# Performance work log

Measured on AMD Instinct MI355X. Metric: run time of the kernel, lower is better.

The kernel has to match this reference:

```python
import jax, jax.numpy as jnp
import numpy as np

DIM = 256; CTX_DIM = 256; K = 7; SK = 5; NH = 4  # num_heads*2
HD = DIM // NH; SCALE = HD ** -0.5
H = 64; W = 64; HC = 56; WC = 56
LN_EPS = 1e-6; BN_EPS = 1e-5


def make_bias_idx(k, h, w):
    # Faithful port of ContMix.generate_idx + apply_rpb index construction.
    rs = 2 * k - 1
    idx_h = np.arange(k); idx_w = np.arange(k)
    idx_k = (idx_h[:, None] * rs + idx_w).reshape(-1)
    rep_h = np.ones(k, np.int64); rep_h[k // 2] = h - (k - 1)
    rep_w = np.ones(k, np.int64); rep_w[k // 2] = w - (k - 1)
    bias_hw = np.repeat(idx_h, rep_h)[:, None] * rs + np.repeat(idx_w, rep_w)  # (h, w)
    bias_idx = (bias_hw[..., None] + idx_k).reshape(-1, k * k)                 # (h*w, k^2)
    return jnp.asarray(bias_idx[::-1].copy())  # torch.flip along dim 0


def window_idx(n, k):
    # NATTEN-style clamped neighborhood window starts.
    s = np.clip(np.arange(n) - k // 2, 0, n - k)
    return jnp.asarray(s[:, None] + np.arange(k))  # (n, k)


BIDX1 = make_bias_idx(SK, H, W)
BIDX2 = make_bias_idx(K, H, W)
IDXI_S = window_idx(H, SK); IDXJ_S = window_idx(W, SK)
IDXI_L = window_idx(H, K);  IDXJ_L = window_idx(W, K)


def ln2d(x, g, b):
    # LayerNorm over channel dim per spatial location, x: (B, C, H, W)
    mu = x.mean(1, keepdims=True)
    var = ((x - mu) ** 2).mean(1, keepdims=True)
    return (x - mu) * jax.lax.rsqrt(var + LN_EPS) * g[None, :, None, None] + b[None, :, None, None]


def conv1x1(x, Wt):
    return jnp.einsum('oc,bchw->bohw', Wt, x)


def apply_rpb(attn, rpb, bias_idx, h, w):
    g = rpb.shape[0]
    r = rpb.reshape(g, -1)[:, bias_idx]  # (g, h*w, k^2)
    return attn + r.reshape(1, g, h, w, -1)


def na2d_av(attn, value, k, idx_i, idx_j):
    # attn: (B, G, H, W, k^2), value: (B, G, H, W, C)
    B, G, h, w, _ = attn.shape
    v = value[:, :, idx_i]        # (B, G, H, k, W, C)
    v = v[:, :, :, :, idx_j]      # (B, G, H, k, W, k, C)
    a = attn.reshape(B, G, h, w, k, k)
    return jnp.einsum('bghwpq,bghpwqc->bghwc', a, v)


def contmix_forward(x, ctx, Wq, gq, bq, Wk, gk, bk, Wproj, rpb1, rpb2, Wdy, bn_g, bn_b):
    B = x.shape[0]
    q = ln2d(conv1x1(x, Wq), gq, bq) * SCALE                       # (B, DIM, H, W)
    # AdaptiveAvgPool2d(7) on 56x56 -> exact 8x8 bins
    kctx = ctx.reshape(B, CTX_DIM, 7, HC // 7, 7, WC // 7).mean((3, 5))
    kf = ln2d(conv1x1(kctx, Wk), gk, bk)                            # (B, DIM, 7, 7)
    q = q.reshape(B, NH, HD, H * W)
    kf = kf.reshape(B, NH, HD, 49)
    wgt = jnp.einsum('bgcn,bgcl->bgnl', q, kf)                      # (B, 4, HW, 49)
    wgt = jnp.einsum('ml,bgnl->bgnm', Wproj, wgt)                   # (B, 4, HW, 74)
    wgt = wgt.reshape(B, NH, H, W, SK * SK + K * K)
    attn1 = wgt[:, :NH // 2, :, :, :SK * SK]                        # group1, 25
    attn2 = wgt[:, NH // 2:, :, :, SK * SK:]                        # group2, 49
    attn1 = jax.nn.softmax(apply_rpb(attn1, rpb1, BIDX1, H, W), -1)
    attn2 = jax.nn.softmax(apply_rpb(attn2, rpb2, BIDX2, H, W), -1)
    # 'b (m g c) h w -> m b g h w c', m=2, g=2
    v = x.reshape(B, 2, NH // 2, HD, H, W).transpose(1, 0, 2, 4, 5, 3)
    x1 = na2d_av(attn1, v[0], SK, IDXI_S, IDXJ_S)                   # (B, 2, H, W, HD)
    x2 = na2d_av(attn2, v[1], K, IDXI_L, IDXJ_L)
    out = jnp.concatenate([x1, x2], axis=1)                         # (B, 4, H, W, HD)
    out = out.transpose(0, 1, 4, 2, 3).reshape(B, DIM, H, W)
    out = conv1x1(out, Wdy)
    # BatchNorm2d in eval mode: running_mean=0, running_var=1
    out = out * (bn_g * jax.lax.rsqrt(jnp.float32(1.0) + BN_EPS))[None, :, None, None] + bn_b[None, :, None, None]
    return out


def setup_inputs() -> dict:
    key = jax.random.key(0)
    ks = jax.random.split(key, 10)
    d = {}
    d['x'] = jax.random.normal(ks[0], (4, DIM, H, W), jnp.float32)
    d['ctx'] = jax.random.normal(ks[1], (4, CTX_DIM, HC, WC), jnp.float32)
    d['Wq'] = jax.random.normal(ks[2], (DIM, DIM), jnp.float32) * 0.02
    d['gq'] = jnp.ones((DIM,), jnp.float32)
    d['bq'] = jnp.zeros((DIM,), jnp.float32)
    d['Wk'] = jax.random.normal(ks[3], (DIM, CTX_DIM), jnp.float32) * 0.02
    d['gk'] = jnp.ones((DIM,), jnp.float32)
    d['bk'] = jnp.zeros((DIM,), jnp.float32)
    d['Wproj'] = jax.random.normal(ks[4], (SK * SK + K * K, 49), jnp.float32) * 0.1
    d['rpb1'] = jax.random.normal(ks[5], (NH // 2, 2 * SK - 1, 2 * SK - 1), jnp.float32) * 0.02
    d['rpb2'] = jax.random.normal(ks[6], (NH // 2, 2 * K - 1, 2 * K - 1), jnp.float32) * 0.02
    d['Wdy'] = jax.random.normal(ks[7], (DIM, DIM), jnp.float32) * 0.02
    d['bn_g'] = jnp.ones((DIM,), jnp.float32)
    d['bn_b'] = jnp.zeros((DIM,), jnp.float32)
    return d


def reference(x, ctx, Wq, gq, bq, Wk, gk, bk, Wproj, rpb1, rpb2, Wdy, bn_g, bn_b):
    return contmix_forward(x, ctx, Wq, gq, bq, Wk, gk, bk, Wproj, rpb1, rpb2, Wdy, bn_g, bn_b)
```

## Files before the change

kernel.cpp:

```cpp
#include <hip/hip_runtime.h>

#define DEV __device__ __forceinline__

typedef __bf16 bf16x8 __attribute__((ext_vector_type(8)));
typedef __bf16 bf16x4 __attribute__((ext_vector_type(4)));
typedef float floatx4 __attribute__((ext_vector_type(4)));

__global__ __launch_bounds__(256)
void prep_kernel(const float* __restrict__ Wq, const float* __restrict__ Wdy,
                 const float* __restrict__ ctx, const float* __restrict__ x,
                 __bf16* __restrict__ wqb, __bf16* __restrict__ wdyb,
                 float* __restrict__ kctx, __bf16* __restrict__ xt) {
  __shared__ float tile[64][65];
  int bid = blockIdx.x, t = threadIdx.x;
  if (bid < 256) {
    int i = bid * 256 + t;
    wqb[i]  = (__bf16)Wq[i];
    wdyb[i] = (__bf16)Wdy[i];
  } else if (bid < 512) {
    int bc = (bid - 256) * 4 + (t >> 6);
    const float* src = ctx + (size_t)bc * (56 * 56);
    int w = t & 63;
#pragma unroll
    for (int pi = 0; pi < 7; ++pi) {
      float s = 0.f;
      if (w < 56) {
#pragma unroll
        for (int di = 0; di < 8; ++di) s += src[(pi * 8 + di) * 56 + w];
      }
      s += __shfl_down(s, 4);
      s += __shfl_down(s, 2);
      s += __shfl_down(s, 1);
      if (w < 56 && (w & 7) == 0)
        kctx[(size_t)bc * 49 + pi * 7 + (w >> 3)] = s * (1.f / 64.f);
    }
  } else {
    int idx = bid - 512;
    int b = idx >> 8, c0 = ((idx >> 6) & 3) * 64, n0 = (idx & 63) * 64;
    int lane = t & 63, rg = t >> 6;
    const float* src = x + ((size_t)b * 256 + c0) * 4096 + n0;
    for (int i = rg; i < 64; i += 4) tile[i][lane] = src[(size_t)i * 4096 + lane];
    __syncthreads();
    __bf16* dst = xt + ((size_t)b * 4096 + n0) * 256 + c0;
    for (int i = rg; i < 64; i += 4) dst[(size_t)i * 256 + lane] = (__bf16)tile[lane][i];
  }
}

__global__ __launch_bounds__(256)
void kf_ln_kernel(const float* __restrict__ kctx, const float* __restrict__ Wk,
                  const float* __restrict__ gk, const float* __restrict__ bk,
                  float* __restrict__ kf) {
  int b = blockIdx.x / 49, l = blockIdx.x % 49;
  __shared__ float xs[256];
  __shared__ float r1[4], r2[4];
  int o = threadIdx.x;
  xs[o] = kctx[((size_t)b * 256 + o) * 49 + l];
  __syncthreads();
  const float* wrow = Wk + (size_t)o * 256;
  float acc = 0.f;
#pragma unroll 8
  for (int c = 0; c < 256; c += 4) {
    float4 wv = *(const float4*)(wrow + c);
    acc += wv.x * xs[c] + wv.y * xs[c + 1] + wv.z * xs[c + 2] + wv.w * xs[c + 3];
  }
  float s1 = acc, s2 = acc * acc;
#pragma unroll
  for (int off = 32; off > 0; off >>= 1) {
    s1 += __shfl_down(s1, off);
    s2 += __shfl_down(s2, off);
  }
  int wv_ = o >> 6, ln = o & 63;
  if (ln == 0) { r1[wv_] = s1; r2[wv_] = s2; }
  __syncthreads();
  float mu  = (r1[0] + r1[1] + r1[2] + r1[3]) * (1.f / 256.f);
  float var = (r2[0] + r2[1] + r2[2] + r2[3]) * (1.f / 256.f) - mu * mu;
  float rstd = rsqrtf(var + 1e-6f);
  kf[((size_t)b * 256 + o) * 49 + l] = (acc - mu) * rstd * gk[o] + bk[o];
}

__global__ __launch_bounds__(256)
void kfp_kernel(const float* __restrict__ kf, const float* __restrict__ Wproj,
                __bf16* __restrict__ kfpT) {
  int bg = blockIdx.x; int b = bg >> 2, g = bg & 3;
  int m0 = blockIdx.y * 16;
  __shared__ float kfs[64][50];
  __shared__ float wps[16][50];
  int t = threadIdx.x;
  for (int i = t; i < 64 * 49; i += 256) {
    int d = i / 49, l = i % 49;
    kfs[d][l] = kf[((size_t)b * 256 + g * 64 + d) * 49 + l];
  }
  for (int i = t; i < 16 * 49; i += 256) {
    int m = i / 49, l = i % 49;
    wps[m][l] = (m0 + m < 74) ? Wproj[(m0 + m) * 49 + l] : 0.f;
  }
  __syncthreads();
  for (int i = t; i < 64 * 16; i += 256) {
    int d = i >> 4, m = i & 15;
    float s = 0.f;
    if (m0 + m < 74) {
#pragma unroll 7
      for (int l = 0; l < 49; ++l) s += kfs[d][l] * wps[m][l];
    }
    kfpT[(size_t)bg * 5120 + (m0 + m) * 64 + d] = (__bf16)s;
  }
}

DEV int rep_idx(int p, int kc, int t1, int sub) {
  return p < kc ? p : (p < t1 ? kc : p - sub);
}

template <int KK>
DEV void softmax_write(const float* wms, const float* rpb_s, __bf16* __restrict__ attnL,
                       int bg, int n_glob, int row) {
  constexpr int CNT = KK * KK;
  constexpr int RS  = 2 * KK - 1;
  constexpr int KC  = KK / 2;
  constexpr int T1  = KC + (64 - KK + 1);
  constexpr int SUB = 64 - KK;
  constexpr int MLO = (KK == 5) ? 0 : 25;
  constexpr int PW  = (KK == 5) ? 32 : 56;
  int h = n_glob >> 6, w = n_glob & 63;
  int rh = rep_idx(63 - h, KC, T1, SUB);
  int rw = rep_idx(63 - w, KC, T1, SUB);
  float vals[CNT];
  float mx = -1e30f;
#pragma unroll
  for (int m = 0; m < CNT; ++m) {
    int ki = m / KK, kj = m % KK;
    float v = wms[row * 81 + MLO + m] + rpb_s[(rh + ki) * RS + rw + kj];
    vals[m] = v; mx = fmaxf(mx, v);
  }
  float ssum = 0.f;
#pragma unroll
  for (int m = 0; m < CNT; ++m) { float e = __expf(vals[m] - mx); vals[m] = e; ssum += e; }
  float inv = 1.f / ssum;
  __bf16 hv[PW];
#pragma unroll
  for (int m = 0; m < PW; ++m) hv[m] = (__bf16)(m < CNT ? vals[m] * inv : 0.f);
  __bf16* ap = attnL + ((size_t)bg * 4096 + n_glob) * 56;
#pragma unroll
  for (int i = 0; i < PW / 8; ++i) *(bf16x8*)(ap + i * 8) = *(bf16x8*)&hv[i * 8];
}

__global__ __launch_bounds__(512, 1)
void qattn_kernel(const __bf16* __restrict__ Wb, const __bf16* __restrict__ XT,
                  const __bf16* __restrict__ kfpT,
                  const float* __restrict__ gq, const float* __restrict__ bq,
                  const float* __restrict__ rpb1, const float* __restrict__ rpb2,
                  __bf16* __restrict__ attnL) {
  __shared__ float wms[256 * 81];
  __shared__ float rpb_s[500];
  __shared__ float gqs[256], bqs[256];
  __shared__ float red_s[4][64], red_q[4][64];
  __shared__ float st_mu[64], st_rs[64];
  __bf16* As  = (__bf16*)wms;
  __bf16* Bs  = (__bf16*)wms + 8192;
  __bf16* Aat = (__bf16*)wms;

  int b  = blockIdx.z;
  int n0 = blockIdx.x * 64;
  int t  = threadIdx.x;
  int lane = t & 63, wv = t >> 6;
  int oq = wv & 3, nh = wv >> 2;
  int col = lane & 15, quad = lane >> 4;

  if (t < 256) {
    gqs[t] = gq[t] * 0.125f;
    bqs[t] = bq[t] * 0.125f;
  }
  for (int i = t; i < 162; i += 512) rpb_s[i] = rpb1[i];
  for (int i = t; i < 338; i += 512) rpb_s[162 + i] = rpb2[i];

  floatx4 acc[4][2];
#pragma unroll
  for (int i = 0; i < 4; ++i)
#pragma unroll
    for (int j = 0; j < 2; ++j) acc[i][j] = {0.f, 0.f, 0.f, 0.f};

  int rowA = t >> 1, halfA = (t & 1) * 16;
  int rowB = t >> 3, kB = (t & 7) * 4;
  const __bf16* wp = Wb + (size_t)rowA * 256 + halfA;
  const __bf16* xp = XT + ((size_t)b * 4096 + n0 + rowB) * 256 + kB;
  bf16x8 ra0 = *(const bf16x8*)wp;
  bf16x8 ra1 = *(const bf16x8*)(wp + 8);
  bf16x4 rb  = *(const bf16x4*)xp;

  for (int c0 = 0; c0 < 256; c0 += 32) {
    *(bf16x8*)&As[rowA * 32 + halfA]     = ra0;
    *(bf16x8*)&As[rowA * 32 + halfA + 8] = ra1;
    *(bf16x4*)&Bs[rowB * 32 + kB]        = rb;
    __syncthreads();
    if (c0 + 32 < 256) {
      ra0 = *(const bf16x8*)(wp + c0 + 32);
      ra1 = *(const bf16x8*)(wp + c0 + 40);
      rb  = *(const bf16x4*)(xp + c0 + 32);
    }
    bf16x8 fa[4], fb[2];
#pragma unroll
    for (int i = 0; i < 4; ++i)
      fa[i] = *(const bf16x8*)&As[(oq * 64 + i * 16 + col) * 32 + quad * 8];
#pragma unroll
    for (int j = 0; j < 2; ++j)
      fb[j] = *(const bf16x8*)&Bs[(nh * 32 + j * 16 + col) * 32 + quad * 8];
#pragma unroll
    for (int i = 0; i < 4; ++i)
#pragma unroll
      for (int j = 0; j < 2; ++j)
        acc[i][j] = __builtin_amdgcn_mfma_f32_16x16x32_bf16(fa[i], fb[j], acc[i][j], 0, 0, 0);
    __syncthreads();
  }

#pragma unroll
  for (int j = 0; j < 2; ++j) {
    float s = 0.f, q = 0.f;
#pragma unroll
    for (int i = 0; i < 4; ++i)
#pragma unroll
      for (int r = 0; r < 4; ++r) { float v = acc[i][j][r]; s += v; q += v * v; }
    s += __shfl_xor(s, 16); s += __shfl_xor(s, 32);
    q += __shfl_xor(q, 16); q += __shfl_xor(q, 32);
    if (quad == 0) {
      red_s[oq][nh * 32 + j * 16 + col] = s;
      red_q[oq][nh * 32 + j * 16 + col] = q;
    }
  }
  __syncthreads();
  if (t < 64) {
    float s = red_s[0][t] + red_s[1][t] + red_s[2][t] + red_s[3][t];
    float q = red_q[0][t] + red_q[1][t] + red_q[2][t] + red_q[3][t];
    float mu  = s * (1.f / 256.f);
    float var = q * (1.f / 256.f) - mu * mu;
    st_mu[t] = mu;
    st_rs[t] = rsqrtf(var + 1e-6f);
  }
  __syncthreads();

#pragma unroll
  for (int j = 0; j < 2; ++j) {
    int n_loc = nh * 32 + j * 16 + col;
    float mu = st_mu[n_loc], rs = st_rs[n_loc];
#pragma unroll
    for (int i = 0; i < 4; ++i) {
      __bf16 pk[4];
#pragma unroll
      for (int r = 0; r < 4; ++r) {
        int o = oq * 64 + i * 16 + quad * 4 + r;
        pk[r] = (__bf16)((acc[i][j][r] - mu) * rs * gqs[o] + bqs[o]);
      }
      *(bf16x4*)&Aat[((size_t)(oq * 64 + n_loc)) * 72 + i * 16 + quad * 4] = *(bf16x4*)pk;
    }
  }
  __syncthreads();

  bf16x8 fa2[2][2], fb2[2][5];
  const __bf16* kp = kfpT + (size_t)(b * 4 + oq) * 5120;
#pragma unroll
  for (int ks = 0; ks < 2; ++ks) {
#pragma unroll
    for (int a = 0; a < 2; ++a)
      fa2[ks][a] = *(const bf16x8*)&Aat[((size_t)(oq * 64 + nh * 32 + a * 16 + col)) * 72 + ks * 32 + quad * 8];
#pragma unroll
    for (int nt = 0; nt < 5; ++nt)
      fb2[ks][nt] = *(const bf16x8*)&kp[(nt * 16 + col) * 64 + ks * 32 + quad * 8];
  }
  floatx4 acc2[2][5];
#pragma unroll
  for (int a = 0; a < 2; ++a)
#pragma unroll
    for (int nt = 0; nt < 5; ++nt) acc2[a][nt] = {0.f, 0.f, 0.f, 0.f};
#pragma unroll
  for (int ks = 0; ks < 2; ++ks)
#pragma unroll
    for (int a = 0; a < 2; ++a)
#pragma unroll
      for (int nt = 0; nt < 5; ++nt)
        acc2[a][nt] = __builtin_amdgcn_mfma_f32_16x16x32_bf16(fa2[ks][a], fb2[ks][nt], acc2[a][nt], 0, 0, 0);
  __syncthreads();

#pragma unroll
  for (int a = 0; a < 2; ++a)
#pragma unroll
    for (int nt = 0; nt < 5; ++nt)
#pragma unroll
      for (int r = 0; r < 4; ++r)
        wms[(oq * 64 + nh * 32 + a * 16 + quad * 4 + r) * 81 + nt * 16 + col] = acc2[a][nt][r];
  __syncthreads();

  if (t < 256) {
    int g2 = t >> 6;
    int n_glob = n0 + (t & 63);
    int bg = b * 4 + g2;
    if (g2 < 2) softmax_write<5>(wms, rpb_s + g2 * 81,              attnL, bg, n_glob, t);
    else        softmax_write<7>(wms, rpb_s + 162 + (g2 - 2) * 169, attnL, bg, n_glob, t);
  }
}

template <int MODE>
__global__ __launch_bounds__(256, 2)
void conv_mfma_kernel(const __bf16* __restrict__ Wb, const __bf16* __restrict__ Xin,
                      void* __restrict__ Yout, float* __restrict__ stats,
                      const float* __restrict__ bn_g, const float* __restrict__ bn_b) {
  int b  = blockIdx.z;
  int n0 = blockIdx.x * 128;
  int o0 = blockIdx.y * 128;
  __shared__ __bf16 As[128 * 32];
  __shared__ __bf16 Bs[128 * 32];
  int t = threadIdx.x;
  int lane = t & 63, wv = t >> 6;
  int mq = (wv & 1) * 64, nq = (wv >> 1) * 64;
  int col = lane & 15, quad = lane >> 4;
  floatx4 acc[4][4];
#pragma unroll
  for (int i = 0; i < 4; ++i)
#pragma unroll
    for (int j = 0; j < 4; ++j) acc[i][j] = {0.f, 0.f, 0.f, 0.f};
  int sm = t >> 1, sk = (t & 1) << 4;
  const __bf16* wp = Wb + (size_t)(o0 + sm) * 256 + sk;
  auto xaddr = [&](int c0) -> const __bf16* {
    if (MODE == 0) {
      return Xin + ((size_t)b * 4096 + n0 + sm) * 256 + c0 + sk;
    } else {
      int c = c0 + sk, g = c >> 6, c64 = c & 63;
      return Xin + (((size_t)(b * 4 + g)) * 4096 + n0 + sm) * 64 + c64;
    }
  };
  bf16x8 wa0 = *(const bf16x8*)wp;
  bf16x8 wa1 = *(const bf16x8*)(wp + 8);
  const __bf16* x0 = xaddr(0);
  bf16x8 xb0 = *(const bf16x8*)x0;
  bf16x8 xb1 = *(const bf16x8*)(x0 + 8);
  for (int c0 = 0; c0 < 256; c0 += 32) {
    *(bf16x8*)&As[sm * 32 + sk]     = wa0;
    *(bf16x8*)&As[sm * 32 + sk + 8] = wa1;
    *(bf16x8*)&Bs[sm * 32 + sk]     = xb0;
    *(bf16x8*)&Bs[sm * 32 + sk + 8] = xb1;
    __syncthreads();
    if (c0 + 32 < 256) {
      wa0 = *(const bf16x8*)(wp + c0 + 32);
      wa1 = *(const bf16x8*)(wp + c0 + 40);
      const __bf16* xn = xaddr(c0 + 32);
      xb0 = *(const bf16x8*)xn;
      xb1 = *(const bf16x8*)(xn + 8);
    }
    bf16x8 fa[4], fb[4];
#pragma unroll
    for (int i = 0; i < 4; ++i)
      fa[i] = *(const bf16x8*)&As[(mq + i * 16 + col) * 32 + quad * 8];
#pragma unroll
    for (int j = 0; j < 4; ++j)
      fb[j] = *(const bf16x8*)&Bs[(nq + j * 16 + col) * 32 + quad * 8];
#pragma unroll
    for (int i = 0; i < 4; ++i)
#pragma unroll
      for (int j = 0; j < 4; ++j)
        acc[i][j] = __builtin_amdgcn_mfma_f32_16x16x32_bf16(fa[i], fb[j], acc[i][j], 0, 0, 0);
    __syncthreads();
  }
  {
    float* Yf = (float*)Yout + (size_t)b * 256 * 4096;
#pragma unroll
    for (int i = 0; i < 4; ++i) {
#pragma unroll
      for (int r = 0; r < 4; ++r) {
        int o = o0 + mq + i * 16 + quad * 4 + r;
        float scale = bn_g[o] * 0.9999950000374997f;
        float shift = bn_b[o];
        float* yrow = Yf + (size_t)o * 4096 + n0 + nq + col;
#pragma unroll
        for (int j = 0; j < 4; ++j) yrow[j * 16] = acc[i][j][r] * scale + shift;
      }
    }
  }
}

template <int KK>
DEV void na2d_body(const __bf16* __restrict__ attnL, const __bf16* __restrict__ XT,
                   __bf16* __restrict__ midT, __bf16* xs, int bg, int h0, int chalf, int t) {
  constexpr int CNT = KK * KK, KC = KK / 2, SMAX = 64 - KK;
  constexpr int ROWS = KK + 3;
  constexpr int PW = (KK == 5) ? 32 : 56;
  int b = bg >> 2, g = bg & 3;
  int si0 = min(max(h0 - KC, 0), SMAX);
  {
    int sn = t >> 2, sc = t & 3;
    const __bf16* src = XT + ((size_t)b * 4096 + sn) * 256 + g * 64 + chalf * 32 + sc * 8;
#pragma unroll
    for (int r = 0; r < ROWS; ++r) {
      int gr = min(si0 + r, 63);
      *(bf16x8*)&xs[(r * 64 + sn) * 40 + sc * 8] = *(const bf16x8*)(src + (size_t)gr * 64 * 256);
    }
  }
  __syncthreads();
  int w = t >> 2, cg = t & 3;
  int sj = min(max(w - KC, 0), SMAX);
#pragma unroll
  for (int h4 = 0; h4 < 4; ++h4) {
    int h = h0 + h4;
    int base = min(max(h - KC, 0), SMAX) - si0;
    bf16x8 avh[PW / 8];
    const __bf16* ap = attnL + ((size_t)bg * 4096 + h * 64 + w) * 56;
#pragma unroll
    for (int i = 0; i < PW / 8; ++i) avh[i] = *(const bf16x8*)(ap + i * 8);
    float av[CNT];
#pragma unroll
    for (int m = 0; m < CNT; ++m) av[m] = (float)avh[m / 8][m % 8];
    float acc[8] = {};
#pragma unroll
    for (int p = 0; p < KK; ++p) {
      const __bf16* xr = &xs[((base + p) * 64 + sj) * 40 + cg * 8];
#pragma unroll
      for (int q = 0; q < KK; ++q) {
        bf16x8 v = *(const bf16x8*)(xr + q * 40);
        float a = av[p * KK + q];
#pragma unroll
        for (int e = 0; e < 8; ++e) acc[e] += a * (float)v[e];
      }
    }
    __bf16 hv[8];
#pragma unroll
    for (int e = 0; e < 8; ++e) hv[e] = (__bf16)acc[e];
    *(bf16x8*)&midT[((size_t)bg * 4096 + h * 64 + w) * 64 + chalf * 32 + cg * 8] = *(bf16x8*)hv;
  }
}

__global__ __launch_bounds__(256)
void na2d_kernel(const __bf16* __restrict__ attnL, const __bf16* __restrict__ XT,
                 __bf16* __restrict__ midT) {
  __shared__ __bf16 xs[10 * 64 * 40];
  int bg = blockIdx.x, h0 = blockIdx.y * 4, chalf = blockIdx.z, t = threadIdx.x;
  if ((bg & 3) < 2) na2d_body<5>(attnL, XT, midT, xs, bg, h0, chalf, t);
  else              na2d_body<7>(attnL, XT, midT, xs, bg, h0, chalf, t);
}

extern "C" void kernel_launch(void* const* d_in, const int* in_sizes, int n_in,
                              void* d_out, int out_size, void* d_ws, size_t ws_size,
                              hipStream_t stream) {
  const float* x     = (const float*)d_in[0];
  const float* ctx   = (const float*)d_in[1];
  const float* Wq    = (const float*)d_in[2];
  const float* gq    = (const float*)d_in[3];
  const float* bq    = (const float*)d_in[4];
  const float* Wk    = (const float*)d_in[5];
  const float* gk    = (const float*)d_in[6];
  const float* bk    = (const float*)d_in[7];
  const float* Wproj = (const float*)d_in[8];
  const float* rpb1  = (const float*)d_in[9];
  const float* rpb2  = (const float*)d_in[10];
  const float* Wdy   = (const float*)d_in[11];
  const float* bn_g  = (const float*)d_in[12];
  const float* bn_b  = (const float*)d_in[13];
  float* out = (float*)d_out;

  float* ws     = (float*)d_ws;
  float* kctx   = ws;
  float* kf     = kctx + 50176;
  __bf16* attnL = (__bf16*)(kf + 50176);
  __bf16* wqb   = attnL + 3670016;
  __bf16* wdyb  = wqb + 65536;
  __bf16* kfpT  = wdyb + 65536;
  __bf16* XT    = kfpT + 81920;
  __bf16* midT  = XT + 4194304;

  prep_kernel<<<dim3(1536), dim3(256), 0, stream>>>(Wq, Wdy, ctx, x, wqb, wdyb, kctx, XT);
  kf_ln_kernel<<<dim3(196), dim3(256), 0, stream>>>(kctx, Wk, gk, bk, kf);
  kfp_kernel<<<dim3(16, 5), dim3(256), 0, stream>>>(kf, Wproj, kfpT);
  qattn_kernel<<<dim3(64, 1, 4), dim3(512), 0, stream>>>(wqb, XT, kfpT, gq, bq, rpb1, rpb2, attnL);
  na2d_kernel<<<dim3(16, 16, 2), dim3(256), 0, stream>>>(attnL, XT, midT);
  conv_mfma_kernel<1><<<dim3(32, 2, 4), dim3(256), 0, stream>>>(wdyb, midT, out, nullptr, bn_g, bn_b);
}
```

Baseline: 160.5 us.

## Enlarge na2d tile to 8 rows and stage values as fp32 in LDS

The neighborhood-attention kernel now processes 8 output rows per block with 512 threads instead of 4 rows with 256. This cuts the halo rows reloaded per output row (14 staged rows for 8 outputs versus 10 for 4). Values are converted from bf16 to fp32 once when staged into shared memory, so the inner loop does float4 loads with no per-element conversion. The thread mapping also changes so consecutive lanes cover consecutive w positions. The costs are doubled LDS bytes per element (about 129KB), a launch bound of one block per CU, and half as many blocks (256), which may reduce latency hiding.

```diff
diff --git a/kernel.cpp b/kernel.cpp
--- a/kernel.cpp
+++ b/kernel.cpp
@@ -375,28 +375,33 @@
 }
 
 template <int KK>
-DEV void na2d_body(const __bf16* __restrict__ attnL, const __bf16* __restrict__ XT,
-                   __bf16* __restrict__ midT, __bf16* xs, int bg, int h0, int chalf, int t) {
+DEV void na2d_body8(const __bf16* __restrict__ attnL, const __bf16* __restrict__ XT,
+                    __bf16* __restrict__ midT, float* xs, int bg, int h0, int chalf, int t) {
   constexpr int CNT = KK * KK, KC = KK / 2, SMAX = 64 - KK;
-  constexpr int ROWS = KK + 3;
+  constexpr int ROWS = KK + 7;
   constexpr int PW = (KK == 5) ? 32 : 56;
   int b = bg >> 2, g = bg & 3;
   int si0 = min(max(h0 - KC, 0), SMAX);
   {
-    int sn = t >> 2, sc = t & 3;
-    const __bf16* src = XT + ((size_t)b * 4096 + sn) * 256 + g * 64 + chalf * 32 + sc * 8;
-#pragma unroll
-    for (int r = 0; r < ROWS; ++r) {
+    int sn = t & 63, sc8 = (t >> 6) & 3, rh = t >> 8;
+    const __bf16* src = XT + ((size_t)b * 4096 + sn) * 256 + g * 64 + chalf * 32 + sc8 * 8;
+    for (int r = rh; r < ROWS; r += 2) {
       int gr = min(si0 + r, 63);
-      *(bf16x8*)&xs[(r * 64 + sn) * 40 + sc * 8] = *(const bf16x8*)(src + (size_t)gr * 64 * 256);
-    }
-  }
-  __syncthreads();
-  int w = t >> 2, cg = t & 3;
+      bf16x8 v = *(const bf16x8*)(src + (size_t)gr * 64 * 256);
+      float f[8];
+#pragma unroll
+      for (int e = 0; e < 8; ++e) f[e] = (float)v[e];
+      float* d = &xs[(r * 64 + sn) * 36 + sc8 * 8];
+      *(float4*)d       = *(float4*)&f[0];
+      *(float4*)(d + 4) = *(float4*)&f[4];
+    }
+  }
+  __syncthreads();
+  int w = t & 63, cg = (t >> 6) & 3, hh = t >> 8;
   int sj = min(max(w - KC, 0), SMAX);
 #pragma unroll
   for (int h4 = 0; h4 < 4; ++h4) {
-    int h = h0 + h4;
+    int h = h0 + hh * 4 + h4;
     int base = min(max(h - KC, 0), SMAX) - si0;
     bf16x8 avh[PW / 8];
     const __bf16* ap = attnL + ((size_t)bg * 4096 + h * 64 + w) * 56;
@@ -408,13 +413,14 @@
     float acc[8] = {};
 #pragma unroll
     for (int p = 0; p < KK; ++p) {
-      const __bf16* xr = &xs[((base + p) * 64 + sj) * 40 + cg * 8];
+      const float* xr = &xs[((base + p) * 64 + sj) * 36 + cg * 8];
 #pragma unroll
       for (int q = 0; q < KK; ++q) {
-        bf16x8 v = *(const bf16x8*)(xr + q * 40);
+        float4 v0 = *(const float4*)(xr + q * 36);
+        float4 v1 = *(const float4*)(xr + q * 36 + 4);
         float a = av[p * KK + q];
-#pragma unroll
-        for (int e = 0; e < 8; ++e) acc[e] += a * (float)v[e];
+        acc[0] += a * v0.x; acc[1] += a * v0.y; acc[2] += a * v0.z; acc[3] += a * v0.w;
+        acc[4] += a * v1.x; acc[5] += a * v1.y; acc[6] += a * v1.z; acc[7] += a * v1.w;
       }
     }
     __bf16 hv[8];
@@ -424,13 +430,13 @@
   }
 }
 
-__global__ __launch_bounds__(256)
+__global__ __launch_bounds__(512, 1)
 void na2d_kernel(const __bf16* __restrict__ attnL, const __bf16* __restrict__ XT,
                  __bf16* __restrict__ midT) {
-  __shared__ __bf16 xs[10 * 64 * 40];
-  int bg = blockIdx.x, h0 = blockIdx.y * 4, chalf = blockIdx.z, t = threadIdx.x;
-  if ((bg & 3) < 2) na2d_body<5>(attnL, XT, midT, xs, bg, h0, chalf, t);
-  else              na2d_body<7>(attnL, XT, midT, xs, bg, h0, chalf, t);
+  __shared__ float xs[14 * 64 * 36];
+  int bg = blockIdx.x, h0 = blockIdx.y * 8, chalf = blockIdx.z, t = threadIdx.x;
+  if ((bg & 3) < 2) na2d_body8<5>(attnL, XT, midT, xs, bg, h0, chalf, t);
+  else              na2d_body8<7>(attnL, XT, midT, xs, bg, h0, chalf, t);
 }
 
 extern "C" void kernel_launch(void* const* d_in, const int* in_sizes, int n_in,
@@ -466,6 +472,6 @@
   kf_ln_kernel<<<dim3(196), dim3(256), 0, stream>>>(kctx, Wk, gk, bk, kf);
   kfp_kernel<<<dim3(16, 5), dim3(256), 0, stream>>>(kf, Wproj, kfpT);
   qattn_kernel<<<dim3(64, 1, 4), dim3(512), 0, stream>>>(wqb, XT, kfpT, gq, bq, rpb1, rpb2, attnL);
-  na2d_kernel<<<dim3(16, 16, 2), dim3(256), 0, stream>>>(attnL, XT, midT);
+  na2d_kernel<<<dim3(16, 8, 2), dim3(512), 0, stream>>>(attnL, XT, midT);
   conv_mfma_kernel<1><<<dim3(32, 2, 4), dim3(256), 0, stream>>>(wdyb, midT, out, nullptr, bn_g, bn_b);
 }
```

After: 157.9 us. No clear change (-1.6%).
